# Kernel tuning notes

Measured on AMD Instinct MI355X. Metric: run time of the kernel, lower is better.

The kernel has to match this reference:

```python
import jax, jax.numpy as jnp
import numpy as np
from jax import lax

NBITS = 8
QMAX_SYM = 2 ** (NBITS - 1) - 1  # 127
QMIN_SYM = -(2 ** (NBITS - 1))   # -128
QMAX_ASYM = 2 ** NBITS - 1       # 255


def fake_quant_sym(x):
    # symmetric per-tensor fake quant with straight-through estimator
    delta = lax.stop_gradient(jnp.max(jnp.abs(x))) / QMAX_SYM + 1e-8
    q = jnp.clip(jnp.round(x / delta), QMIN_SYM, QMAX_SYM) * delta
    return x + lax.stop_gradient(q - x)


def fake_quant_asym(x):
    # asymmetric per-tensor fake quant (for softmax output) with STE
    xmin = lax.stop_gradient(jnp.min(x))
    xmax = lax.stop_gradient(jnp.max(x))
    delta = (xmax - xmin) / QMAX_ASYM + 1e-8
    zp = jnp.round(-xmin / delta)
    q = (jnp.clip(jnp.round(x / delta) + zp, 0, QMAX_ASYM) - zp) * delta
    return x + lax.stop_gradient(q - x)


def layer_norm(x, g, b, eps=1e-5):
    mu = jnp.mean(x, axis=-1, keepdims=True)
    var = jnp.var(x, axis=-1, keepdims=True)
    return (x - mu) * lax.rsqrt(var + eps) * g + b


def setup_inputs() -> dict:
    key = jax.random.key(0)
    ks = jax.random.split(key, 8)
    B, N, C = 8, 4096, 256
    s = 0.02
    return {
        "x": jax.random.normal(ks[0], (B, N, C), jnp.float32),
        "q_w": jax.random.normal(ks[1], (C, C), jnp.float32) * s,
        "q_b": jnp.zeros((C,), jnp.float32),
        "kv_w": jax.random.normal(ks[2], (2 * C, C), jnp.float32) * s,
        "kv_b": jnp.zeros((2 * C,), jnp.float32),
        "sr_w": jax.random.normal(ks[3], (C, C, 4, 4), jnp.float32) * s,
        "sr_b": jnp.zeros((C,), jnp.float32),
        "norm_g": jnp.ones((C,), jnp.float32),
        "norm_b": jnp.zeros((C,), jnp.float32),
        "proj_w": jax.random.normal(ks[4], (C, C), jnp.float32) * s,
        "proj_b": jnp.zeros((C,), jnp.float32),
        "H": 64,
        "W": 64,
    }


def reference(x, q_w, q_b, kv_w, kv_b, sr_w, sr_b, norm_g, norm_b, proj_w, proj_b, H, W):
    B, N, C = x.shape
    num_heads = 8
    sr_ratio = 4
    dh = C // num_heads
    scale = dh ** -0.5

    # weight fake-quant (PreQuantModule, sym=True)
    q_wq = fake_quant_sym(q_w)
    kv_wq = fake_quant_sym(kv_w)
    sr_wq = fake_quant_sym(sr_w)
    proj_wq = fake_quant_sym(proj_w)

    # q projection -> [B, heads, N, dh], post-act sym fake quant
    q = (jnp.einsum('bnc,dc->bnd', x, q_wq) + q_b)
    q = fake_quant_sym(q.reshape(B, N, num_heads, dh).transpose(0, 2, 1, 3))

    # spatial reduction: x -> [B,C,H,W], conv k=stride=sr_ratio, then LayerNorm
    x_ = x.transpose(0, 2, 1).reshape(B, C, H, W)
    x_ = lax.conv_general_dilated(x_, sr_wq, (sr_ratio, sr_ratio), 'VALID',
                                  dimension_numbers=('NCHW', 'OIHW', 'NCHW'))
    x_ = x_ + sr_b[None, :, None, None]
    N2 = (H // sr_ratio) * (W // sr_ratio)
    x_ = x_.reshape(B, C, N2).transpose(0, 2, 1)  # [B, N2, C]
    x_ = layer_norm(x_, norm_g, norm_b)

    # kv projection -> k, v [B, heads, N2, dh], post-act sym fake quant
    kv = jnp.einsum('bnc,dc->bnd', x_, kv_wq) + kv_b
    kv = kv.reshape(B, N2, 2, num_heads, dh).transpose(2, 0, 3, 1, 4)
    k = fake_quant_sym(kv[0])
    v = fake_quant_sym(kv[1])

    # attention with asym fake quant on softmax output
    attn = jnp.einsum('bhnd,bhmd->bhnm', q, k) * scale
    attn = jax.nn.softmax(attn, axis=-1)
    attn = fake_quant_asym(attn)

    out = jnp.einsum('bhnm,bhmd->bhnd', attn, v)
    out = out.transpose(0, 2, 1, 3).reshape(B, N, C)
    out = jnp.einsum('bnc,dc->bnd', out, proj_wq) + proj_b
    return out
```

## Files before the change

### kernel.cpp

```cpp
#include <hip/hip_runtime.h>
#include <stdint.h>

typedef float f32x4 __attribute__((ext_vector_type(4)));
typedef __bf16 bf16x8 __attribute__((ext_vector_type(8)));

#define DEV __device__ __forceinline__

DEV unsigned short f2bf(float f) {
  unsigned u = __float_as_uint(f);
  u += 0x7FFFu + ((u >> 16) & 1u);
  return (unsigned short)(u >> 16);
}

DEV float exp2_(float x) {
#if __has_builtin(__builtin_amdgcn_exp2f)
  return __builtin_amdgcn_exp2f(x);
#else
  return exp2f(x);
#endif
}

DEV unsigned cvtpk(float lo, float hi) {
  unsigned r;
  asm("v_cvt_pk_bf16_f32 %0, %1, %2" : "=v"(r) : "v"(lo), "v"(hi));
  return r;
}

DEV void pl32swap(unsigned &a, unsigned &b) {
#if __has_builtin(__builtin_amdgcn_permlane32_swap)
  auto r = __builtin_amdgcn_permlane32_swap(a, b, false, false);
  a = r[0]; b = r[1];
#else
  asm("v_permlane32_swap_b32 %0, %1" : "+v"(a), "+v"(b));
#endif
}

DEV void pl16swap(unsigned &a, unsigned &b) {
#if __has_builtin(__builtin_amdgcn_permlane16_swap)
  auto r = __builtin_amdgcn_permlane16_swap(a, b, false, false);
  a = r[0]; b = r[1];
#else
  asm("v_permlane16_swap_b32 %0, %1" : "+v"(a), "+v"(b));
#endif
}

DEV bf16x8 qfrag(uint4 w, float idq, float dq) {
  unsigned o[4];
  const unsigned* wi = &w.x;
  #pragma unroll
  for (int i = 0; i < 4; i++) {
    float lo = __uint_as_float(wi[i] << 16);
    float hi = __uint_as_float(wi[i] & 0xffff0000u);
    lo = fminf(fmaxf(rintf(lo * idq), -128.f), 127.f) * dq;
    hi = fminf(fmaxf(rintf(hi * idq), -128.f), 127.f) * dq;
    o[i] = cvtpk(lo, hi);
  }
  uint4 r = make_uint4(o[0], o[1], o[2], o[3]);
  return *(bf16x8*)&r;
}

__global__ void k_init(float* scal) {
  int t = threadIdx.x;
  if (t < 16) scal[t] = (t == 7) ? __uint_as_float(0x7f800000u) : 0.f;
}

__global__ __launch_bounds__(256) void k_absmax4(const float* w0, const float* w1,
                                                 const float* w2, const float* w3, float* scal) {
  const float* srcs[4] = {w0, w1, w2, w3};
  const int ns[4] = {65536, 131072, 1048576, 65536};
  int t = blockIdx.y;
  const float* src = srcs[t];
  int n = ns[t];
  float m = 0.f;
  for (int i = blockIdx.x * 256 + threadIdx.x; i < n; i += gridDim.x * 256)
    m = fmaxf(m, fabsf(src[i]));
  #pragma unroll
  for (int d = 1; d < 64; d <<= 1) m = fmaxf(m, __shfl_xor(m, d, 64));
  __shared__ float red[4];
  if ((threadIdx.x & 63) == 0) red[threadIdx.x >> 6] = m;
  __syncthreads();
  if (threadIdx.x == 0) {
    m = fmaxf(fmaxf(red[0], red[1]), fmaxf(red[2], red[3]));
    atomicMax((unsigned*)(scal + t), __float_as_uint(m));
  }
}

__global__ __launch_bounds__(256) void k_quantw(const float* qw, const float* kvw,
                                                const float* prw, const float* srw,
                                                const float* xf,
                                                unsigned short* qo, unsigned short* kvo,
                                                unsigned short* pro, unsigned short* sro,
                                                unsigned short* xbo,
                                                const float* scal) {
  int bx = blockIdx.x;
  int tid = bx * 256 + threadIdx.x;
  {
    int oo = tid >> 12;
    int rem = tid & 4095;
    int khkw = rem >> 8;
    int i = rem & 255;
    float delta = scal[2] / 127.f + 1e-8f;
    float x = srw[oo * 4096 + i * 16 + khkw];
    sro[tid] = f2bf(fminf(fmaxf(rintf(x / delta), -128.f), 127.f) * delta);
  }
  {
    const float4* xs = (const float4*)(xf + (size_t)tid * 8);
    float4 v0 = xs[0], v1 = xs[1];
    unsigned w0 = ((unsigned)f2bf(v0.y) << 16) | f2bf(v0.x);
    unsigned w1 = ((unsigned)f2bf(v0.w) << 16) | f2bf(v0.z);
    unsigned w2 = ((unsigned)f2bf(v1.y) << 16) | f2bf(v1.x);
    unsigned w3 = ((unsigned)f2bf(v1.w) << 16) | f2bf(v1.z);
    *(uint4*)(xbo + (size_t)tid * 8) = make_uint4(w0, w1, w2, w3);
  }
  if (bx < 512) {
    float delta = scal[1] / 127.f + 1e-8f;
    kvo[tid] = f2bf(fminf(fmaxf(rintf(kvw[tid] / delta), -128.f), 127.f) * delta);
  }
  if (bx < 256) {
    float dq = scal[0] / 127.f + 1e-8f;
    qo[tid] = f2bf(fminf(fmaxf(rintf(qw[tid] / dq), -128.f), 127.f) * dq);
    float dp = scal[3] / 127.f + 1e-8f;
    pro[tid] = f2bf(fminf(fmaxf(rintf(prw[tid] / dp), -128.f), 127.f) * dp);
  }
}

__global__ __launch_bounds__(256) void k_gemm_bk(const unsigned short* __restrict__ Ab,
                                                 const unsigned short* __restrict__ W,
                                                 const float* __restrict__ bias,
                                                 float* __restrict__ C,
                                                 int M, int N, float* max_ptr, int split) {
  __shared__ unsigned short As[64 * 136];
  __shared__ unsigned short Bs[64 * 136];
  const int m0 = blockIdx.y * 64, n0 = blockIdx.x * 64;
  const int tid = threadIdx.x;
  const int wid = tid >> 6, lane = tid & 63;
  const int quad = lane >> 4, lr = lane & 15;
  const int wm = wid >> 1, wn = wid & 1;
  f32x4 acc[2][2] = {};
  for (int kb = 0; kb < 256; kb += 128) {
    __syncthreads();
    #pragma unroll
    for (int i = 0; i < 4; i++) {
      int c = i * 256 + tid;
      int row = c >> 4, cu = (c & 15) * 8;
      *(uint4*)&As[row * 136 + cu] = *(const uint4*)(Ab + (size_t)(m0 + row) * 256 + kb + cu);
      *(uint4*)&Bs[row * 136 + cu] = *(const uint4*)(W + (size_t)(n0 + row) * 256 + kb + cu);
    }
    __syncthreads();
    #pragma unroll
    for (int kc = 0; kc < 4; kc++) {
      bf16x8 af0 = *(const bf16x8*)&As[(wm * 32 + lr) * 136 + kc * 32 + quad * 8];
      bf16x8 af1 = *(const bf16x8*)&As[(wm * 32 + 16 + lr) * 136 + kc * 32 + quad * 8];
      bf16x8 bf0 = *(const bf16x8*)&Bs[(wn * 32 + lr) * 136 + kc * 32 + quad * 8];
      bf16x8 bf1 = *(const bf16x8*)&Bs[(wn * 32 + 16 + lr) * 136 + kc * 32 + quad * 8];
      acc[0][0] = __builtin_amdgcn_mfma_f32_16x16x32_bf16(af0, bf0, acc[0][0], 0, 0, 0);
      acc[0][1] = __builtin_amdgcn_mfma_f32_16x16x32_bf16(af0, bf1, acc[0][1], 0, 0, 0);
      acc[1][0] = __builtin_amdgcn_mfma_f32_16x16x32_bf16(af1, bf0, acc[1][0], 0, 0, 0);
      acc[1][1] = __builtin_amdgcn_mfma_f32_16x16x32_bf16(af1, bf1, acc[1][1], 0, 0, 0);
    }
  }
  float amax = 0.f;
  #pragma unroll
  for (int mi = 0; mi < 2; mi++)
    #pragma unroll
    for (int ni = 0; ni < 2; ni++) {
      int col = n0 + wn * 32 + ni * 16 + lr;
      float bv = bias[col];
      #pragma unroll
      for (int r = 0; r < 4; r++) {
        int row = m0 + wm * 32 + mi * 16 + quad * 4 + r;
        float v = acc[mi][ni][r] + bv;
        C[(size_t)row * N + col] = v;
        amax = fmaxf(amax, fabsf(v));
      }
    }
  if (max_ptr) {
    #pragma unroll
    for (int d = 1; d < 64; d <<= 1) amax = fmaxf(amax, __shfl_xor(amax, d, 64));
    if (lane == 0) {
      int slot = (split > 0 && n0 >= split) ? 1 : 0;
      atomicMax((unsigned*)(max_ptr + slot), __float_as_uint(amax));
    }
  }
}

template<int MODE>
__global__ __launch_bounds__(256) void k_gemm128(const unsigned short* __restrict__ Ab,
                                                 const unsigned short* __restrict__ W,
                                                 const float* __restrict__ bias,
                                                 void* __restrict__ Cout,
                                                 float* max_ptr) {
  __shared__ unsigned short As[128 * 72];
  __shared__ unsigned short Bs[128 * 72];
  const int id = blockIdx.x;
  const int xcd = id & 7, idx = id >> 3;
  const int mt = xcd * 32 + (idx >> 1), nt = idx & 1;
  const int m0 = mt * 128, n0 = nt * 128;
  const int tid = threadIdx.x;
  const int wid = tid >> 6, lane = tid & 63;
  const int quad = lane >> 4, lr = lane & 15;
  const int wm = wid >> 1, wn = wid & 1;
  f32x4 acc[4][4] = {};
  for (int kb = 0; kb < 256; kb += 64) {
    __syncthreads();
    #pragma unroll
    for (int i = 0; i < 4; i++) {
      int c = i * 256 + tid;
      int row = c >> 3, cu = (c & 7) * 8;
      *(uint4*)&As[row * 72 + cu] = *(const uint4*)(Ab + (size_t)(m0 + row) * 256 + kb + cu);
      *(uint4*)&Bs[row * 72 + cu] = *(const uint4*)(W + (size_t)(n0 + row) * 256 + kb + cu);
    }
    __syncthreads();
    #pragma unroll
    for (int kc = 0; kc < 2; kc++) {
      bf16x8 af[4], bf[4];
      #pragma unroll
      for (int mi = 0; mi < 4; mi++)
        af[mi] = *(const bf16x8*)&As[(wm * 64 + mi * 16 + lr) * 72 + kc * 32 + quad * 8];
      #pragma unroll
      for (int ni = 0; ni < 4; ni++)
        bf[ni] = *(const bf16x8*)&Bs[(wn * 64 + ni * 16 + lr) * 72 + kc * 32 + quad * 8];
      #pragma unroll
      for (int mi = 0; mi < 4; mi++)
        #pragma unroll
        for (int ni = 0; ni < 4; ni++)
          acc[mi][ni] = __builtin_amdgcn_mfma_f32_16x16x32_bf16(af[mi], bf[ni], acc[mi][ni], 0, 0, 0);
    }
  }
  float amax = 0.f;
  #pragma unroll
  for (int mi = 0; mi < 4; mi++)
    #pragma unroll
    for (int ni = 0; ni < 4; ni++) {
      int col = n0 + wn * 64 + ni * 16 + lr;
      float bv = bias[col];
      #pragma unroll
      for (int r = 0; r < 4; r++) {
        int row = m0 + wm * 64 + mi * 16 + quad * 4 + r;
        float v = acc[mi][ni][r] + bv;
        if (MODE == 0) {
          ((float*)Cout)[(size_t)row * 256 + col] = v;
        } else {
          int b = row >> 12, nn = row & 4095;
          int h = col >> 5, j = col & 31;
          ((unsigned short*)Cout)[((size_t)(b * 8 + h) * 4096 + nn) * 32 + j] = f2bf(v);
        }
        amax = fmaxf(amax, fabsf(v));
      }
    }
  if (max_ptr) {
    #pragma unroll
    for (int d = 1; d < 64; d <<= 1) amax = fmaxf(amax, __shfl_xor(amax, d, 64));
    if (lane == 0) atomicMax((unsigned*)max_ptr, __float_as_uint(amax));
  }
}

__global__ __launch_bounds__(256) void k_conv_sk(const unsigned short* __restrict__ xb,
                                                 const unsigned short* __restrict__ W,
                                                 float* __restrict__ C) {
  __shared__ unsigned short As[64 * 136];
  __shared__ unsigned short Bs[64 * 136];
  const int id = blockIdx.x;
  const int xcd = id & 7, idx = id >> 3;
  const int a = idx >> 2, nt = idx & 3;
  const int ag = xcd * 16 + a;
  const int mt = ag & 31, z = ag >> 5;
  const int m0 = mt * 64, n0 = nt * 64;
  const int kOff = z * 1024;
  C += (size_t)z * 2048 * 256;
  const int tid = threadIdx.x;
  const int wid = tid >> 6, lane = tid & 63;
  const int quad = lane >> 4, lr = lane & 15;
  const int wm = wid >> 1, wn = wid & 1;
  f32x4 acc[2][2] = {};
  for (int kb = 0; kb < 1024; kb += 128) {
    __syncthreads();
    #pragma unroll
    for (int i = 0; i < 4; i++) {
      int c = i * 256 + tid;
      int row = c >> 4, cu = (c & 15) * 8;
      int kk = kOff + kb + cu;
      int m = m0 + row;
      int b = m >> 8, p = m & 255, ph = p >> 4, pw = p & 15;
      int q = kk >> 8, ii = kk & 255;
      int n = (ph * 4 + (q >> 2)) * 64 + pw * 4 + (q & 3);
      *(uint4*)&As[row * 136 + cu] = *(const uint4*)(xb + ((size_t)(b * 4096 + n) * 256 + ii));
      *(uint4*)&Bs[row * 136 + cu] = *(const uint4*)(W + (size_t)(n0 + row) * 4096 + kk);
    }
    __syncthreads();
    #pragma unroll
    for (int kc = 0; kc < 4; kc++) {
      bf16x8 af0 = *(const bf16x8*)&As[(wm * 32 + lr) * 136 + kc * 32 + quad * 8];
      bf16x8 af1 = *(const bf16x8*)&As[(wm * 32 + 16 + lr) * 136 + kc * 32 + quad * 8];
      bf16x8 bf0 = *(const bf16x8*)&Bs[(wn * 32 + lr) * 136 + kc * 32 + quad * 8];
      bf16x8 bf1 = *(const bf16x8*)&Bs[(wn * 32 + 16 + lr) * 136 + kc * 32 + quad * 8];
      acc[0][0] = __builtin_amdgcn_mfma_f32_16x16x32_bf16(af0, bf0, acc[0][0], 0, 0, 0);
      acc[0][1] = __builtin_amdgcn_mfma_f32_16x16x32_bf16(af0, bf1, acc[0][1], 0, 0, 0);
      acc[1][0] = __builtin_amdgcn_mfma_f32_16x16x32_bf16(af1, bf0, acc[1][0], 0, 0, 0);
      acc[1][1] = __builtin_amdgcn_mfma_f32_16x16x32_bf16(af1, bf1, acc[1][1], 0, 0, 0);
    }
  }
  #pragma unroll
  for (int mi = 0; mi < 2; mi++)
    #pragma unroll
    for (int ni = 0; ni < 2; ni++) {
      int col = n0 + wn * 32 + ni * 16 + lr;
      #pragma unroll
      for (int r = 0; r < 4; r++) {
        int row = m0 + wm * 32 + mi * 16 + quad * 4 + r;
        C[(size_t)row * 256 + col] = acc[mi][ni][r];
      }
    }
}

__global__ __launch_bounds__(256) void k_ln(const float* __restrict__ convp, const float* srb,
                                            const float* g, const float* bb,
                                            unsigned short* __restrict__ xn) {
  int row = blockIdx.x, c = threadIdx.x;
  float v = srb[c];
  #pragma unroll
  for (int s = 0; s < 4; s++) v += convp[s * 524288 + row * 256 + c];
  __shared__ float red[4];
  float s = v;
  #pragma unroll
  for (int d = 1; d < 64; d <<= 1) s += __shfl_xor(s, d, 64);
  if ((c & 63) == 0) red[c >> 6] = s;
  __syncthreads();
  float mu = (red[0] + red[1] + red[2] + red[3]) * (1.f / 256.f);
  __syncthreads();
  float dv = v - mu;
  float s2 = dv * dv;
  #pragma unroll
  for (int d = 1; d < 64; d <<= 1) s2 += __shfl_xor(s2, d, 64);
  if ((c & 63) == 0) red[c >> 6] = s2;
  __syncthreads();
  float var = (red[0] + red[1] + red[2] + red[3]) * (1.f / 256.f);
  float rs = 1.f / sqrtf(var + 1e-5f);
  xn[row * 256 + c] = f2bf(dv * rs * g[c] + bb[c]);
}

__global__ __launch_bounds__(256) void k_quant_kv(const float* __restrict__ kv,
                                                  unsigned short* __restrict__ kq,
                                                  unsigned short* __restrict__ vqt,
                                                  const float* scal) {
  int tid4 = blockIdx.x * 256 + threadIdx.x;
  int i4 = tid4 * 4;
  int row = i4 >> 9, d0 = i4 & 511;
  int b = row >> 8, n2 = row & 255;
  int t = d0 >> 8, hj = d0 & 255;
  int h = hj >> 5, j = hj & 31;
  float delta = scal[5 + t] / 127.f + 1e-8f;
  float4 v = *(const float4*)(kv + i4);
  unsigned short r0 = f2bf(fminf(fmaxf(rintf(v.x / delta), -128.f), 127.f) * delta);
  unsigned short r1 = f2bf(fminf(fmaxf(rintf(v.y / delta), -128.f), 127.f) * delta);
  unsigned short r2 = f2bf(fminf(fmaxf(rintf(v.z / delta), -128.f), 127.f) * delta);
  unsigned short r3 = f2bf(fminf(fmaxf(rintf(v.w / delta), -128.f), 127.f) * delta);
  if (t == 0) {
    ushort4 rr = make_ushort4(r0, r1, r2, r3);
    *(ushort4*)(kq + ((size_t)((b * 8 + h) * 256 + n2) * 32) + j) = rr;
  } else {
    size_t base = (size_t)(b * 8 + h) * 32 * 256 + n2;
    vqt[base + (size_t)(j + 0) * 256] = r0;
    vqt[base + (size_t)(j + 1) * 256] = r1;
    vqt[base + (size_t)(j + 2) * 256] = r2;
    vqt[base + (size_t)(j + 3) * 256] = r3;
  }
}

__global__ __launch_bounds__(256) void k_attn1(const unsigned short* __restrict__ qq,
                                               const unsigned short* __restrict__ kq,
                                               float2* __restrict__ rowstats,
                                               float* scal) {
  __shared__ unsigned short KsL[8192];
  __shared__ float red[8];
  const int bh = blockIdx.y;
  const int row0 = blockIdx.x * 256;
  const int tid = threadIdx.x, wid = tid >> 6, lane = tid & 63, quad = lane >> 4, lr = lane & 15;
  const float c2 = 0.17677669529663687f * 1.4426950408889634f;
  const unsigned short* kb = kq + (size_t)bh * 8192;
  #pragma unroll
  for (int k = 0; k < 4; k++) {
    int cid = k * 256 + tid;
    int seg = cid >> 6, lc = cid & 63, qc = lc >> 4, lrc = lc & 15;
    *(uint4*)&KsL[cid * 8] = *(const uint4*)(kb + (seg * 16 + lrc) * 32 + qc * 8);
  }
  float dq = scal[4] / 127.f + 1e-8f;
  float idq = 1.f / dq;
  __syncthreads();
  float wmin = 1e30f, wmax = 0.f;
  #pragma unroll
  for (int g = 0; g < 4; g++) {
    int rowg = row0 + g * 64 + wid * 16 + lr;
    uint4 qw = *(const uint4*)(qq + ((size_t)bh * 4096 + rowg) * 32 + quad * 8);
    bf16x8 qf = qfrag(qw, idq, dq);
    f32x4 acc[16] = {};
    #pragma unroll
    for (int t = 0; t < 16; t++) {
      bf16x8 kf = *(const bf16x8*)&KsL[(t * 64 + quad * 16 + lr) * 8];
      acc[t] = __builtin_amdgcn_mfma_f32_16x16x32_bf16(kf, qf, acc[t], 0, 0, 0);
    }
    float mxr = -1e30f, mnr = 1e30f;
    #pragma unroll
    for (int t = 0; t < 16; t++)
      #pragma unroll
      for (int r = 0; r < 4; r++) {
        float s = acc[t][r];
        mxr = fmaxf(mxr, s); mnr = fminf(mnr, s);
      }
    #pragma unroll
    for (int d = 16; d < 64; d <<= 1) {
      mxr = fmaxf(mxr, __shfl_xor(mxr, d, 64));
      mnr = fminf(mnr, __shfl_xor(mnr, d, 64));
    }
    float m2 = mxr * c2;
    float l = 0.f;
    #pragma unroll
    for (int t = 0; t < 16; t++)
      #pragma unroll
      for (int r = 0; r < 4; r++)
        l += exp2_(fmaf(acc[t][r], c2, -m2));
    #pragma unroll
    for (int d = 16; d < 64; d <<= 1) l += __shfl_xor(l, d, 64);
    float inv_l = 1.f / l;
    if (lane < 16)
      rowstats[(size_t)bh * 4096 + rowg] = make_float2(m2, inv_l);
    wmax = fmaxf(wmax, inv_l);
    wmin = fminf(wmin, exp2_((mnr - mxr) * c2) * inv_l);
  }
  #pragma unroll
  for (int d = 1; d < 16; d <<= 1) {
    wmax = fmaxf(wmax, __shfl_xor(wmax, d, 64));
    wmin = fminf(wmin, __shfl_xor(wmin, d, 64));
  }
  if (lane == 0) { red[wid] = wmin; red[4 + wid] = wmax; }
  __syncthreads();
  if (tid == 0) {
    float mn = fminf(fminf(red[0], red[1]), fminf(red[2], red[3]));
    float mx = fmaxf(fmaxf(red[4], red[5]), fmaxf(red[6], red[7]));
    atomicMin((unsigned*)(scal + 7), __float_as_uint(mn));
    atomicMax((unsigned*)(scal + 8), __float_as_uint(mx));
  }
}

__global__ __launch_bounds__(256) void k_attn2(const unsigned short* __restrict__ qq,
                                               const unsigned short* __restrict__ kq,
                                               const unsigned short* __restrict__ vqt,
                                               const float* scal,
                                               const float2* __restrict__ rowstats,
                                               unsigned short* __restrict__ attn_out) {
  __shared__ unsigned short KsL[8192];
  __shared__ unsigned short VsL[8192];
  const int bh = blockIdx.y, b = bh >> 3, h = bh & 7;
  const int row0 = blockIdx.x * 256;
  const int tid = threadIdx.x, wid = tid >> 6, lane = tid & 63, quad = lane >> 4, lr = lane & 15;
  const float c2 = 0.17677669529663687f * 1.4426950408889634f;
  const unsigned short* kb = kq + (size_t)bh * 8192;
  const unsigned short* vb = vqt + (size_t)bh * 8192;
  #pragma unroll
  for (int k = 0; k < 4; k++) {
    int cid = k * 256 + tid;
    int seg = cid >> 6, lc = cid & 63, qc = lc >> 4, lrc = lc & 15;
    *(uint4*)&KsL[cid * 8] = *(const uint4*)(kb + (seg * 16 + lrc) * 32 + qc * 8);
    *(uint4*)&VsL[cid * 8] =
        *(const uint4*)(vb + ((seg & 1) * 16 + lrc) * 256 + (seg >> 1) * 32 + qc * 8);
  }
  float dq = scal[4] / 127.f + 1e-8f;
  float idq = 1.f / dq;
  float pmin = scal[7], pmax = scal[8];
  float delta = (pmax - pmin) / 255.f + 1e-8f;
  float zp = rintf(-pmin / delta);
  float qlo = -zp, qhi = 255.f - zp;
  __syncthreads();
  #pragma unroll
  for (int g = 0; g < 4; g++) {
    int rowg = row0 + g * 64 + wid * 16 + lr;
    uint4 qw = *(const uint4*)(qq + ((size_t)bh * 4096 + rowg) * 32 + quad * 8);
    bf16x8 qf = qfrag(qw, idq, dq);
    float2 st = rowstats[(size_t)bh * 4096 + rowg];
    f32x4 acc[16] = {};
    #pragma unroll
    for (int t = 0; t < 16; t++) {
      bf16x8 kf = *(const bf16x8*)&KsL[(t * 64 + quad * 16 + lr) * 8];
      acc[t] = __builtin_amdgcn_mfma_f32_16x16x32_bf16(kf, qf, acc[t], 0, 0, 0);
    }
    float ofs = __log2f(st.y / delta) - st.x;
    f32x4 o0 = {}, o1 = {};
    #pragma unroll
    for (int ks = 0; ks < 8; ks++) {
      float pv[8];
      #pragma unroll
      for (int half = 0; half < 2; half++) {
        #pragma unroll
        for (int r = 0; r < 4; r++) {
          float v = exp2_(fmaf(acc[2 * ks + half][r], c2, ofs));
          pv[half * 4 + r] = fminf(fmaxf(rintf(v), qlo), qhi) * delta;
        }
      }
      unsigned wa = cvtpk(pv[0], pv[1]);
      unsigned wb = cvtpk(pv[2], pv[3]);
      unsigned wc = cvtpk(pv[4], pv[5]);
      unsigned wd = cvtpk(pv[6], pv[7]);
      pl32swap(wa, wc);
      pl16swap(wa, wc);
      pl32swap(wb, wd);
      pl16swap(wb, wd);
      uint4 w = make_uint4(wa, wb, wc, wd);
      bf16x8 pa = *(bf16x8*)&w;
      bf16x8 b0 = *(const bf16x8*)&VsL[((ks * 2 + 0) * 64 + quad * 16 + lr) * 8];
      bf16x8 b1 = *(const bf16x8*)&VsL[((ks * 2 + 1) * 64 + quad * 16 + lr) * 8];
      o0 = __builtin_amdgcn_mfma_f32_16x16x32_bf16(pa, b0, o0, 0, 0, 0);
      o1 = __builtin_amdgcn_mfma_f32_16x16x32_bf16(pa, b1, o1, 0, 0, 0);
    }
    #pragma unroll
    for (int r = 0; r < 4; r++) {
      int n = row0 + g * 64 + wid * 16 + quad * 4 + r;
      size_t base = ((size_t)(b * 4096) + n) * 256 + h * 32;
      attn_out[base + lr] = f2bf(o0[r]);
      attn_out[base + 16 + lr] = f2bf(o1[r]);
    }
  }
}

extern "C" void kernel_launch(void* const* d_in, const int* in_sizes, int n_in,
                              void* d_out, int out_size, void* d_ws, size_t ws_size,
                              hipStream_t stream) {
  const float* x      = (const float*)d_in[0];
  const float* q_w    = (const float*)d_in[1];
  const float* q_b    = (const float*)d_in[2];
  const float* kv_w   = (const float*)d_in[3];
  const float* kv_b   = (const float*)d_in[4];
  const float* sr_w   = (const float*)d_in[5];
  const float* sr_b   = (const float*)d_in[6];
  const float* norm_g = (const float*)d_in[7];
  const float* norm_b = (const float*)d_in[8];
  const float* proj_w = (const float*)d_in[9];
  const float* proj_b = (const float*)d_in[10];
  float* out = (float*)d_out;

  char* ws = (char*)d_ws;
  float* scal = (float*)ws;
  unsigned short* q_wq    = (unsigned short*)(ws + 256);
  unsigned short* kv_wq   = (unsigned short*)(ws + 131328);
  unsigned short* proj_wq = (unsigned short*)(ws + 393472);
  unsigned short* sr_wq   = (unsigned short*)(ws + 524544);
  unsigned short* xn      = (unsigned short*)(ws + 2621696);
  float*          kv_f    = (float*)(ws + 3670272);
  unsigned short* kq      = (unsigned short*)(ws + 7864576);
  unsigned short* vqt     = (unsigned short*)(ws + 8913152);
  float2*         rowstats= (float2*)(ws + 9961728);
  float*          convp   = (float*)(ws + 12058880);
  unsigned short* attn_o  = (unsigned short*)(ws + 12058880);
  unsigned short* qq      = (unsigned short*)(ws + 45613312);
  unsigned short* xb      = (unsigned short*)(ws + 62390528);

  k_init<<<1, 64, 0, stream>>>(scal);
  k_absmax4<<<dim3(64, 4), 256, 0, stream>>>(q_w, kv_w, sr_w, proj_w, scal);
  k_quantw<<<4096, 256, 0, stream>>>(q_w, kv_w, proj_w, sr_w, x,
                                     q_wq, kv_wq, proj_wq, sr_wq, xb, scal);
  k_conv_sk<<<512, 256, 0, stream>>>(xb, sr_wq, convp);
  k_ln<<<2048, 256, 0, stream>>>(convp, sr_b, norm_g, norm_b, xn);
  k_gemm_bk<<<dim3(8, 32), 256, 0, stream>>>(xn, kv_wq, kv_b, kv_f, 2048, 512, scal + 5, 256);
  k_gemm128<1><<<512, 256, 0, stream>>>(xb, q_wq, q_b, qq, scal + 4);
  k_quant_kv<<<1024, 256, 0, stream>>>(kv_f, kq, vqt, scal);
  k_attn1<<<dim3(16, 64), 256, 0, stream>>>(qq, kq, rowstats, scal);
  k_attn2<<<dim3(16, 64), 256, 0, stream>>>(qq, kq, vqt, scal, rowstats, attn_o);
  k_gemm128<0><<<512, 256, 0, stream>>>(attn_o, proj_wq, proj_b, out, nullptr);
}
```

Baseline: 277.3 us.

## Merge KV and Q projection GEMMs into one launch and quantize K/V in attention

Combines the KV projection GEMM and the Q projection GEMM into a single kernel launch, with block ranges selecting the branch. The KV branch now writes bf16 K and transposed V directly in the per-head layouts, which removes the fp32 kv buffer and the separate k_quant_kv kernel. The symmetric fake-quant of K and V moves into the attention kernels' shared-memory load path. In exchange, each attention block re-quantizes K/V on load, K/V are rounded to bf16 before quantization, and the V writes from the GEMM epilogue are strided.

```diff
diff --git a/kernel.cpp b/kernel.cpp
--- a/kernel.cpp
+++ b/kernel.cpp
@@ -44,7 +44,7 @@
 #endif
 }
 
-DEV bf16x8 qfrag(uint4 w, float idq, float dq) {
+DEV uint4 qfrag4(uint4 w, float idq, float dq) {
   unsigned o[4];
   const unsigned* wi = &w.x;
   #pragma unroll
@@ -55,7 +55,11 @@
     hi = fminf(fmaxf(rintf(hi * idq), -128.f), 127.f) * dq;
     o[i] = cvtpk(lo, hi);
   }
-  uint4 r = make_uint4(o[0], o[1], o[2], o[3]);
+  return make_uint4(o[0], o[1], o[2], o[3]);
+}
+
+DEV bf16x8 qfrag(uint4 w, float idq, float dq) {
+  uint4 r = qfrag4(w, idq, dq);
   return *(bf16x8*)&r;
 }
 
@@ -124,72 +128,133 @@
   }
 }
 
-__global__ __launch_bounds__(256) void k_gemm_bk(const unsigned short* __restrict__ Ab,
-                                                 const unsigned short* __restrict__ W,
-                                                 const float* __restrict__ bias,
-                                                 float* __restrict__ C,
-                                                 int M, int N, float* max_ptr, int split) {
-  __shared__ unsigned short As[64 * 136];
-  __shared__ unsigned short Bs[64 * 136];
-  const int m0 = blockIdx.y * 64, n0 = blockIdx.x * 64;
+__global__ __launch_bounds__(256) void k_gemm_qkv(const unsigned short* __restrict__ xnrm,
+                                                  const unsigned short* __restrict__ kvw,
+                                                  const float* __restrict__ kvb,
+                                                  const unsigned short* __restrict__ xb,
+                                                  const unsigned short* __restrict__ qw,
+                                                  const float* __restrict__ qb,
+                                                  unsigned short* __restrict__ kqu,
+                                                  unsigned short* __restrict__ vqtu,
+                                                  unsigned short* __restrict__ qq,
+                                                  float* scal) {
+  __shared__ unsigned short smem[18432];
   const int tid = threadIdx.x;
   const int wid = tid >> 6, lane = tid & 63;
   const int quad = lane >> 4, lr = lane & 15;
   const int wm = wid >> 1, wn = wid & 1;
-  f32x4 acc[2][2] = {};
-  for (int kb = 0; kb < 256; kb += 128) {
-    __syncthreads();
-    #pragma unroll
-    for (int i = 0; i < 4; i++) {
-      int c = i * 256 + tid;
-      int row = c >> 4, cu = (c & 15) * 8;
-      *(uint4*)&As[row * 136 + cu] = *(const uint4*)(Ab + (size_t)(m0 + row) * 256 + kb + cu);
-      *(uint4*)&Bs[row * 136 + cu] = *(const uint4*)(W + (size_t)(n0 + row) * 256 + kb + cu);
-    }
-    __syncthreads();
-    #pragma unroll
-    for (int kc = 0; kc < 4; kc++) {
-      bf16x8 af0 = *(const bf16x8*)&As[(wm * 32 + lr) * 136 + kc * 32 + quad * 8];
-      bf16x8 af1 = *(const bf16x8*)&As[(wm * 32 + 16 + lr) * 136 + kc * 32 + quad * 8];
-      bf16x8 bf0 = *(const bf16x8*)&Bs[(wn * 32 + lr) * 136 + kc * 32 + quad * 8];
-      bf16x8 bf1 = *(const bf16x8*)&Bs[(wn * 32 + 16 + lr) * 136 + kc * 32 + quad * 8];
-      acc[0][0] = __builtin_amdgcn_mfma_f32_16x16x32_bf16(af0, bf0, acc[0][0], 0, 0, 0);
-      acc[0][1] = __builtin_amdgcn_mfma_f32_16x16x32_bf16(af0, bf1, acc[0][1], 0, 0, 0);
-      acc[1][0] = __builtin_amdgcn_mfma_f32_16x16x32_bf16(af1, bf0, acc[1][0], 0, 0, 0);
-      acc[1][1] = __builtin_amdgcn_mfma_f32_16x16x32_bf16(af1, bf1, acc[1][1], 0, 0, 0);
-    }
-  }
-  float amax = 0.f;
-  #pragma unroll
-  for (int mi = 0; mi < 2; mi++)
-    #pragma unroll
-    for (int ni = 0; ni < 2; ni++) {
-      int col = n0 + wn * 32 + ni * 16 + lr;
-      float bv = bias[col];
-      #pragma unroll
-      for (int r = 0; r < 4; r++) {
-        int row = m0 + wm * 32 + mi * 16 + quad * 4 + r;
-        float v = acc[mi][ni][r] + bv;
-        C[(size_t)row * N + col] = v;
-        amax = fmaxf(amax, fabsf(v));
-      }
-    }
-  if (max_ptr) {
+  if (blockIdx.x < 256) {
+    unsigned short* As = smem;
+    unsigned short* Bs = smem + 8704;
+    const int n0 = (blockIdx.x & 7) * 64, m0 = (blockIdx.x >> 3) * 64;
+    f32x4 acc[2][2] = {};
+    for (int kb = 0; kb < 256; kb += 128) {
+      __syncthreads();
+      #pragma unroll
+      for (int i = 0; i < 4; i++) {
+        int c = i * 256 + tid;
+        int row = c >> 4, cu = (c & 15) * 8;
+        *(uint4*)&As[row * 136 + cu] = *(const uint4*)(xnrm + (size_t)(m0 + row) * 256 + kb + cu);
+        *(uint4*)&Bs[row * 136 + cu] = *(const uint4*)(kvw + (size_t)(n0 + row) * 256 + kb + cu);
+      }
+      __syncthreads();
+      #pragma unroll
+      for (int kc = 0; kc < 4; kc++) {
+        bf16x8 af0 = *(const bf16x8*)&As[(wm * 32 + lr) * 136 + kc * 32 + quad * 8];
+        bf16x8 af1 = *(const bf16x8*)&As[(wm * 32 + 16 + lr) * 136 + kc * 32 + quad * 8];
+        bf16x8 bf0 = *(const bf16x8*)&Bs[(wn * 32 + lr) * 136 + kc * 32 + quad * 8];
+        bf16x8 bf1 = *(const bf16x8*)&Bs[(wn * 32 + 16 + lr) * 136 + kc * 32 + quad * 8];
+        acc[0][0] = __builtin_amdgcn_mfma_f32_16x16x32_bf16(af0, bf0, acc[0][0], 0, 0, 0);
+        acc[0][1] = __builtin_amdgcn_mfma_f32_16x16x32_bf16(af0, bf1, acc[0][1], 0, 0, 0);
+        acc[1][0] = __builtin_amdgcn_mfma_f32_16x16x32_bf16(af1, bf0, acc[1][0], 0, 0, 0);
+        acc[1][1] = __builtin_amdgcn_mfma_f32_16x16x32_bf16(af1, bf1, acc[1][1], 0, 0, 0);
+      }
+    }
+    float amax = 0.f;
+    #pragma unroll
+    for (int mi = 0; mi < 2; mi++)
+      #pragma unroll
+      for (int ni = 0; ni < 2; ni++) {
+        int col = n0 + wn * 32 + ni * 16 + lr;
+        float bv = kvb[col];
+        #pragma unroll
+        for (int r = 0; r < 4; r++) {
+          int row = m0 + wm * 32 + mi * 16 + quad * 4 + r;
+          float v = acc[mi][ni][r] + bv;
+          int b = row >> 8, n2 = row & 255;
+          int h = (col >> 5) & 7, j = col & 31;
+          if (col < 256)
+            kqu[((size_t)((b * 8 + h) * 256 + n2)) * 32 + j] = f2bf(v);
+          else
+            vqtu[((size_t)((b * 8 + h) * 32 + j)) * 256 + n2] = f2bf(v);
+          amax = fmaxf(amax, fabsf(v));
+        }
+      }
     #pragma unroll
     for (int d = 1; d < 64; d <<= 1) amax = fmaxf(amax, __shfl_xor(amax, d, 64));
-    if (lane == 0) {
-      int slot = (split > 0 && n0 >= split) ? 1 : 0;
-      atomicMax((unsigned*)(max_ptr + slot), __float_as_uint(amax));
-    }
-  }
-}
-
-template<int MODE>
+    if (lane == 0)
+      atomicMax((unsigned*)(scal + 5 + (n0 >= 256 ? 1 : 0)), __float_as_uint(amax));
+  } else {
+    unsigned short* As = smem;
+    unsigned short* Bs = smem + 9216;
+    const int id = blockIdx.x - 256;
+    const int xcd = id & 7, idx = id >> 3;
+    const int mt = xcd * 32 + (idx >> 1), nt = idx & 1;
+    const int m0 = mt * 128, n0 = nt * 128;
+    f32x4 acc[4][4] = {};
+    for (int kb = 0; kb < 256; kb += 64) {
+      __syncthreads();
+      #pragma unroll
+      for (int i = 0; i < 4; i++) {
+        int c = i * 256 + tid;
+        int row = c >> 3, cu = (c & 7) * 8;
+        *(uint4*)&As[row * 72 + cu] = *(const uint4*)(xb + (size_t)(m0 + row) * 256 + kb + cu);
+        *(uint4*)&Bs[row * 72 + cu] = *(const uint4*)(qw + (size_t)(n0 + row) * 256 + kb + cu);
+      }
+      __syncthreads();
+      #pragma unroll
+      for (int kc = 0; kc < 2; kc++) {
+        bf16x8 af[4], bf[4];
+        #pragma unroll
+        for (int mi = 0; mi < 4; mi++)
+          af[mi] = *(const bf16x8*)&As[(wm * 64 + mi * 16 + lr) * 72 + kc * 32 + quad * 8];
+        #pragma unroll
+        for (int ni = 0; ni < 4; ni++)
+          bf[ni] = *(const bf16x8*)&Bs[(wn * 64 + ni * 16 + lr) * 72 + kc * 32 + quad * 8];
+        #pragma unroll
+        for (int mi = 0; mi < 4; mi++)
+          #pragma unroll
+          for (int ni = 0; ni < 4; ni++)
+            acc[mi][ni] = __builtin_amdgcn_mfma_f32_16x16x32_bf16(af[mi], bf[ni], acc[mi][ni], 0, 0, 0);
+      }
+    }
+    float amax = 0.f;
+    #pragma unroll
+    for (int mi = 0; mi < 4; mi++)
+      #pragma unroll
+      for (int ni = 0; ni < 4; ni++) {
+        int col = n0 + wn * 64 + ni * 16 + lr;
+        float bv = qb[col];
+        #pragma unroll
+        for (int r = 0; r < 4; r++) {
+          int row = m0 + wm * 64 + mi * 16 + quad * 4 + r;
+          float v = acc[mi][ni][r] + bv;
+          int b = row >> 12, nn = row & 4095;
+          int h = col >> 5, j = col & 31;
+          qq[((size_t)(b * 8 + h) * 4096 + nn) * 32 + j] = f2bf(v);
+          amax = fmaxf(amax, fabsf(v));
+        }
+      }
+    #pragma unroll
+    for (int d = 1; d < 64; d <<= 1) amax = fmaxf(amax, __shfl_xor(amax, d, 64));
+    if (lane == 0) atomicMax((unsigned*)(scal + 4), __float_as_uint(amax));
+  }
+}
+
 __global__ __launch_bounds__(256) void k_gemm128(const unsigned short* __restrict__ Ab,
                                                  const unsigned short* __restrict__ W,
                                                  const float* __restrict__ bias,
-                                                 void* __restrict__ Cout,
-                                                 float* max_ptr) {
+                                                 float* __restrict__ C) {
   __shared__ unsigned short As[128 * 72];
   __shared__ unsigned short Bs[128 * 72];
   const int id = blockIdx.x;
@@ -227,7 +292,6 @@
           acc[mi][ni] = __builtin_amdgcn_mfma_f32_16x16x32_bf16(af[mi], bf[ni], acc[mi][ni], 0, 0, 0);
     }
   }
-  float amax = 0.f;
   #pragma unroll
   for (int mi = 0; mi < 4; mi++)
     #pragma unroll
@@ -237,22 +301,9 @@
       #pragma unroll
       for (int r = 0; r < 4; r++) {
         int row = m0 + wm * 64 + mi * 16 + quad * 4 + r;
-        float v = acc[mi][ni][r] + bv;
-        if (MODE == 0) {
-          ((float*)Cout)[(size_t)row * 256 + col] = v;
-        } else {
-          int b = row >> 12, nn = row & 4095;
-          int h = col >> 5, j = col & 31;
-          ((unsigned short*)Cout)[((size_t)(b * 8 + h) * 4096 + nn) * 32 + j] = f2bf(v);
-        }
-        amax = fmaxf(amax, fabsf(v));
-      }
-    }
-  if (max_ptr) {
-    #pragma unroll
-    for (int d = 1; d < 64; d <<= 1) amax = fmaxf(amax, __shfl_xor(amax, d, 64));
-    if (lane == 0) atomicMax((unsigned*)max_ptr, __float_as_uint(amax));
-  }
+        C[(size_t)row * 256 + col] = acc[mi][ni][r] + bv;
+      }
+    }
 }
 
 __global__ __launch_bounds__(256) void k_conv_sk(const unsigned short* __restrict__ xb,
@@ -339,36 +390,8 @@
   xn[row * 256 + c] = f2bf(dv * rs * g[c] + bb[c]);
 }
 
-__global__ __launch_bounds__(256) void k_quant_kv(const float* __restrict__ kv,
-                                                  unsigned short* __restrict__ kq,
-                                                  unsigned short* __restrict__ vqt,
-                                                  const float* scal) {
-  int tid4 = blockIdx.x * 256 + threadIdx.x;
-  int i4 = tid4 * 4;
-  int row = i4 >> 9, d0 = i4 & 511;
-  int b = row >> 8, n2 = row & 255;
-  int t = d0 >> 8, hj = d0 & 255;
-  int h = hj >> 5, j = hj & 31;
-  float delta = scal[5 + t] / 127.f + 1e-8f;
-  float4 v = *(const float4*)(kv + i4);
-  unsigned short r0 = f2bf(fminf(fmaxf(rintf(v.x / delta), -128.f), 127.f) * delta);
-  unsigned short r1 = f2bf(fminf(fmaxf(rintf(v.y / delta), -128.f), 127.f) * delta);
-  unsigned short r2 = f2bf(fminf(fmaxf(rintf(v.z / delta), -128.f), 127.f) * delta);
-  unsigned short r3 = f2bf(fminf(fmaxf(rintf(v.w / delta), -128.f), 127.f) * delta);
-  if (t == 0) {
-    ushort4 rr = make_ushort4(r0, r1, r2, r3);
-    *(ushort4*)(kq + ((size_t)((b * 8 + h) * 256 + n2) * 32) + j) = rr;
-  } else {
-    size_t base = (size_t)(b * 8 + h) * 32 * 256 + n2;
-    vqt[base + (size_t)(j + 0) * 256] = r0;
-    vqt[base + (size_t)(j + 1) * 256] = r1;
-    vqt[base + (size_t)(j + 2) * 256] = r2;
-    vqt[base + (size_t)(j + 3) * 256] = r3;
-  }
-}
-
 __global__ __launch_bounds__(256) void k_attn1(const unsigned short* __restrict__ qq,
-                                               const unsigned short* __restrict__ kq,
+                                               const unsigned short* __restrict__ kqu,
                                                float2* __restrict__ rowstats,
                                                float* scal) {
   __shared__ unsigned short KsL[8192];
@@ -377,15 +400,18 @@
   const int row0 = blockIdx.x * 256;
   const int tid = threadIdx.x, wid = tid >> 6, lane = tid & 63, quad = lane >> 4, lr = lane & 15;
   const float c2 = 0.17677669529663687f * 1.4426950408889634f;
-  const unsigned short* kb = kq + (size_t)bh * 8192;
+  const unsigned short* kb = kqu + (size_t)bh * 8192;
+  float dk = scal[5] / 127.f + 1e-8f;
+  float idk = 1.f / dk;
+  float dq = scal[4] / 127.f + 1e-8f;
+  float idq = 1.f / dq;
   #pragma unroll
   for (int k = 0; k < 4; k++) {
     int cid = k * 256 + tid;
     int seg = cid >> 6, lc = cid & 63, qc = lc >> 4, lrc = lc & 15;
-    *(uint4*)&KsL[cid * 8] = *(const uint4*)(kb + (seg * 16 + lrc) * 32 + qc * 8);
-  }
-  float dq = scal[4] / 127.f + 1e-8f;
-  float idq = 1.f / dq;
+    uint4 kw = *(const uint4*)(kb + (seg * 16 + lrc) * 32 + qc * 8);
+    *(uint4*)&KsL[cid * 8] = qfrag4(kw, idk, dk);
+  }
   __syncthreads();
   float wmin = 1e30f, wmax = 0.f;
   #pragma unroll
@@ -443,8 +469,8 @@
 }
 
 __global__ __launch_bounds__(256) void k_attn2(const unsigned short* __restrict__ qq,
-                                               const unsigned short* __restrict__ kq,
-                                               const unsigned short* __restrict__ vqt,
+                                               const unsigned short* __restrict__ kqu,
+                                               const unsigned short* __restrict__ vqtu,
                                                const float* scal,
                                                const float2* __restrict__ rowstats,
                                                unsigned short* __restrict__ attn_out) {
@@ -454,18 +480,23 @@
   const int row0 = blockIdx.x * 256;
   const int tid = threadIdx.x, wid = tid >> 6, lane = tid & 63, quad = lane >> 4, lr = lane & 15;
   const float c2 = 0.17677669529663687f * 1.4426950408889634f;
-  const unsigned short* kb = kq + (size_t)bh * 8192;
-  const unsigned short* vb = vqt + (size_t)bh * 8192;
+  const unsigned short* kb = kqu + (size_t)bh * 8192;
+  const unsigned short* vb = vqtu + (size_t)bh * 8192;
+  float dk = scal[5] / 127.f + 1e-8f;
+  float idk = 1.f / dk;
+  float dv = scal[6] / 127.f + 1e-8f;
+  float idv = 1.f / dv;
+  float dq = scal[4] / 127.f + 1e-8f;
+  float idq = 1.f / dq;
   #pragma unroll
   for (int k = 0; k < 4; k++) {
     int cid = k * 256 + tid;
     int seg = cid >> 6, lc = cid & 63, qc = lc >> 4, lrc = lc & 15;
-    *(uint4*)&KsL[cid * 8] = *(const uint4*)(kb + (seg * 16 + lrc) * 32 + qc * 8);
-    *(uint4*)&VsL[cid * 8] =
-        *(const uint4*)(vb + ((seg & 1) * 16 + lrc) * 256 + (seg >> 1) * 32 + qc * 8);
-  }
-  float dq = scal[4] / 127.f + 1e-8f;
-  float idq = 1.f / dq;
+    uint4 kw = *(const uint4*)(kb + (seg * 16 + lrc) * 32 + qc * 8);
+    *(uint4*)&KsL[cid * 8] = qfrag4(kw, idk, dk);
+    uint4 vw = *(const uint4*)(vb + ((seg & 1) * 16 + lrc) * 256 + (seg >> 1) * 32 + qc * 8);
+    *(uint4*)&VsL[cid * 8] = qfrag4(vw, idv, dv);
+  }
   float pmin = scal[7], pmax = scal[8];
   float delta = (pmax - pmin) / 255.f + 1e-8f;
   float zp = rintf(-pmin / delta);
@@ -544,9 +575,8 @@
   unsigned short* proj_wq = (unsigned short*)(ws + 393472);
   unsigned short* sr_wq   = (unsigned short*)(ws + 524544);
   unsigned short* xn      = (unsigned short*)(ws + 2621696);
-  float*          kv_f    = (float*)(ws + 3670272);
-  unsigned short* kq      = (unsigned short*)(ws + 7864576);
-  unsigned short* vqt     = (unsigned short*)(ws + 8913152);
+  unsigned short* kqu     = (unsigned short*)(ws + 7864576);
+  unsigned short* vqtu    = (unsigned short*)(ws + 8913152);
   float2*         rowstats= (float2*)(ws + 9961728);
   float*          convp   = (float*)(ws + 12058880);
   unsigned short* attn_o  = (unsigned short*)(ws + 12058880);
@@ -559,10 +589,9 @@
                                      q_wq, kv_wq, proj_wq, sr_wq, xb, scal);
   k_conv_sk<<<512, 256, 0, stream>>>(xb, sr_wq, convp);
   k_ln<<<2048, 256, 0, stream>>>(convp, sr_b, norm_g, norm_b, xn);
-  k_gemm_bk<<<dim3(8, 32), 256, 0, stream>>>(xn, kv_wq, kv_b, kv_f, 2048, 512, scal + 5, 256);
-  k_gemm128<1><<<512, 256, 0, stream>>>(xb, q_wq, q_b, qq, scal + 4);
-  k_quant_kv<<<1024, 256, 0, stream>>>(kv_f, kq, vqt, scal);
-  k_attn1<<<dim3(16, 64), 256, 0, stream>>>(qq, kq, rowstats, scal);
-  k_attn2<<<dim3(16, 64), 256, 0, stream>>>(qq, kq, vqt, scal, rowstats, attn_o);
-  k_gemm128<0><<<512, 256, 0, stream>>>(attn_o, proj_wq, proj_b, out, nullptr);
-}
+  k_gemm_qkv<<<768, 256, 0, stream>>>(xn, kv_wq, kv_b, xb, q_wq, q_b,
+                                      kqu, vqtu, qq, scal);
+  k_attn1<<<dim3(16, 64), 256, 0, stream>>>(qq, kqu, rowstats, scal);
+  k_attn2<<<dim3(16, 64), 256, 0, stream>>>(qq, kqu, vqtu, scal, rowstats, attn_o);
+  k_gemm128<<<512, 256, 0, stream>>>(attn_o, proj_wq, proj_b, out);
+}
```

After: 272.3 us. No clear change (-1.8%).
